# Optimization experiments

Measured on AMD Instinct MI355X. Metric: run time of the kernel, lower is better.

The kernel has to match this reference:

```python
import jax, jax.numpy as jnp
import numpy as np

STATE_LEN = 512
DIM_KEY = 128


def _rope(t, offset):
    # t: (b, h, s, d) -> rotate-half RoPE with given position offset
    b, h, s, d = t.shape
    inv_freq = 1.0 / (10000.0 ** (jnp.arange(0, d, 2, dtype=jnp.float32) / d))
    pos = jnp.arange(s, dtype=jnp.float32) + offset
    ang = pos[:, None] * inv_freq[None, :]            # (s, d/2)
    cos = jnp.concatenate([jnp.cos(ang), jnp.cos(ang)], axis=-1)  # (s, d)
    sin = jnp.concatenate([jnp.sin(ang), jnp.sin(ang)], axis=-1)
    t1, t2 = t[..., : d // 2], t[..., d // 2 :]
    rot = jnp.concatenate([-t2, t1], axis=-1)
    return t * cos + rot * sin


def _proj(x, w):
    # StackedLinear: mixes heads and features. x: (b,h,s,d), w: (h_in,h_out,d_in,d_out)
    return jnp.einsum('bhsd,hgde->bgse', x, w)


def setup_inputs() -> dict:
    key = jax.random.key(0)
    ks = jax.random.split(key, 10)
    x = jax.random.normal(ks[0], (2, 8, 3072, 128), dtype=jnp.float32)
    wshape = (8, 8, 128, 128)
    names = ['Wq', 'Wk', 'Wv', 'Wqs', 'Wks', 'Wvs', 'Wqe', 'Wke', 'Wve']
    inp = {'x': x}
    for i, n in enumerate(names):
        inp[n] = jax.random.normal(ks[i + 1], wshape, dtype=jnp.float32) * 0.02
    inp['offset'] = 0
    return inp


def reference(x, Wq, Wk, Wv, Wqs, Wks, Wvs, Wqe, Wke, Wve, offset):
    # extract_state: front state, middle, end state along seq axis
    xs = x[:, :, :STATE_LEN]
    xm = x[:, :, STATE_LEN:-STATE_LEN]
    xe = x[:, :, -STATE_LEN:]

    q = jnp.concatenate([_proj(xs, Wqs), _proj(xm, Wq), _proj(xe, Wqe)], axis=2)
    k = jnp.concatenate([_proj(xs, Wks), _proj(xm, Wk), _proj(xe, Wke)], axis=2)
    v = jnp.concatenate([_proj(xs, Wvs), _proj(xm, Wv), _proj(xe, Wve)], axis=2)

    q = _rope(q, offset)
    k = _rope(k, offset)

    scores = jnp.einsum('bhqd,bhkd->bhqk', q, k) / (DIM_KEY ** 0.5)
    s = scores.shape[-1]
    mask = jnp.tril(jnp.ones((s, s), dtype=bool))
    scores = jnp.where(mask[None, None], scores, -jnp.inf)
    att = jax.nn.softmax(scores, axis=-1)
    return jnp.einsum('bhqk,bhkd->bhqd', att, v)
```

## Files before the change

### kernel.cpp

```cpp
#include <hip/hip_runtime.h>
#include <hip/hip_bf16.h>
#include <stdint.h>


typedef __bf16   bf16x8 __attribute__((ext_vector_type(8)));
typedef float    f32x4  __attribute__((ext_vector_type(4)));
typedef uint32_t u32x4  __attribute__((ext_vector_type(4)));
typedef uint32_t u32x2  __attribute__((ext_vector_type(2)));
typedef uint16_t u16x4  __attribute__((ext_vector_type(4)));

struct f2 { float c, s; };

#define SEQ   3072
#define NFRQ  64

__device__ const uint8_t TQT[84] = {
  3,4,5,6, 7,7,8,8,9,9,10,10, 11,11,11,12,12,12,13,13,13,14,14,14,
  15,15,15,15,16,16,16,16,17,17,17,17,18,18,18,18,
  19,19,19,19,19,20,20,20,20,20,21,21,21,21,21,22,22,22,22,22,
  23,23,23,23,23,23, 2,6,10,14,18,22, 1,5,9,13,17,21, 0,4,8,12,16,20 };
__device__ const uint8_t TC[84] = {
  0,0,0,0, 0,1,0,1,0,1,0,1, 0,1,2,0,1,2,0,1,2,0,1,2,
  0,1,2,3,0,1,2,3,0,1,2,3,0,1,2,3,
  0,1,2,3,4,0,1,2,3,4,0,1,2,3,4,0,1,2,3,4,
  0,1,2,3,4,5, 0,1,2,3,4,5, 0,1,2,3,4,5, 0,1,2,3,4,5 };
__device__ const uint8_t PT[24]  = {0,0,0,0,0,1,2,3,4,6,8,10,12,15,18,21,24,28,32,36,40,45,50,55};
__device__ const uint8_t CCT[24] = {0,1,2,3,4,6,8,10,12,15,18,21,24,28,32,36,40,45,50,55,60,66,72,78};

static __device__ __forceinline__ uint16_t f2bf(float f) {
  union { float f; uint32_t u; } v; v.f = f;
  uint32_t r = (v.u + 0x7FFFu + ((v.u >> 16) & 1u)) >> 16;
  return (uint16_t)r;
}
static __device__ __forceinline__ float bf2f(uint16_t u) {
  union { uint32_t u; float f; } v; v.u = ((uint32_t)u) << 16;
  return v.f;
}
static __device__ __forceinline__ bf16x8 ldlds(const uint16_t* base, int byteoff) {
  u32x4 t = *reinterpret_cast<const u32x4*>(reinterpret_cast<const char*>(base) + byteoff);
  return __builtin_bit_cast(bf16x8, t);
}
static __device__ __forceinline__ bf16x8 ldglb(const uint16_t* p) {
  u32x4 t = *reinterpret_cast<const u32x4*>(p);
  return __builtin_bit_cast(bf16x8, t);
}

__global__ __launch_bounds__(256) void rope_table_kernel(f2* tab, const int* offp) {
  int i = blockIdx.x * 256 + threadIdx.x;
  if (i >= SEQ * NFRQ) return;
  int s = i >> 6, f = i & 63;
  float pos = (float)(s + offp[0]);
  float inv = powf(10000.0f, -(float)(2 * f) / 128.0f);
  float ang = pos * inv;
  tab[i].c = cosf(ang);
  tab[i].s = sinf(ang);
}

__global__ __launch_bounds__(256) void conv_x_kernel(const float* __restrict__ x,
                                                     uint16_t* __restrict__ xb) {
  int i = blockIdx.x * 256 + threadIdx.x;
  int d4 = i & 31;
  int t  = i >> 5;
  int s  = t % 3072;
  int bh = t / 3072;
  int h  = bh & 7, b = bh >> 3;
  f32x4 v = reinterpret_cast<const f32x4*>(x)[i];
  u16x4 o = { f2bf(v[0]), f2bf(v[1]), f2bf(v[2]), f2bf(v[3]) };
  size_t dst = ((size_t)(b * 3072 + s)) * 1024 + h * 128 + d4 * 4;
  *reinterpret_cast<u16x4*>(xb + dst) = o;
}

__global__ __launch_bounds__(256) void trans_w_kernel(
    const float* W0, const float* W1, const float* W2,
    const float* W3, const float* W4, const float* W5,
    const float* W6, const float* W7, const float* W8,
    uint16_t* __restrict__ Wt) {
  const float* Wall[9] = { W0, W1, W2, W3, W4, W5, W6, W7, W8 };
  int blk  = blockIdx.x;
  int widx = blk >> 6;
  int hg   = blk & 63;
  int h = hg >> 3, g = hg & 7;
  int qkv = widx / 3, seg = widx % 3;
  int sel = (seg == 0) ? (3 + qkv) : ((seg == 1) ? qkv : (6 + qkv));
  const float* src = Wall[sel] + (((size_t)h * 8 + g) * 128) * 128;
  uint16_t* dst = Wt + (((size_t)widx * 8 + g) * 128) * 1024 + h * 128;

  __shared__ uint16_t T[128 * 129];
  int tid = threadIdx.x;
  #pragma unroll
  for (int i = 0; i < 16; ++i) {
    int idx = tid + i * 256;
    int d = idx >> 5, e4 = idx & 31;
    f32x4 v = *reinterpret_cast<const f32x4*>(src + d * 128 + e4 * 4);
    int base = d * 129 + e4 * 4;
    T[base + 0] = f2bf(v[0]); T[base + 1] = f2bf(v[1]);
    T[base + 2] = f2bf(v[2]); T[base + 3] = f2bf(v[3]);
  }
  __syncthreads();
  #pragma unroll
  for (int i = 0; i < 8; ++i) {
    int idx = tid + i * 256;
    int e = idx >> 4, c = idx & 15, d0 = c * 8;
    uint32_t w0 = (uint32_t)T[(d0 + 0) * 129 + e] | ((uint32_t)T[(d0 + 1) * 129 + e] << 16);
    uint32_t w1 = (uint32_t)T[(d0 + 2) * 129 + e] | ((uint32_t)T[(d0 + 3) * 129 + e] << 16);
    uint32_t w2 = (uint32_t)T[(d0 + 4) * 129 + e] | ((uint32_t)T[(d0 + 5) * 129 + e] << 16);
    uint32_t w3 = (uint32_t)T[(d0 + 6) * 129 + e] | ((uint32_t)T[(d0 + 7) * 129 + e] << 16);
    u32x4 o = { w0, w1, w2, w3 };
    *reinterpret_cast<u32x4*>(dst + (size_t)e * 1024 + d0) = o;
  }
}

__global__ __launch_bounds__(256) void proj_kernel(
    const uint16_t* __restrict__ xb, const uint16_t* __restrict__ Wt,
    const f2* __restrict__ rtab,
    uint16_t* __restrict__ qb, uint16_t* __restrict__ kb,
    uint16_t* __restrict__ vtb) {
  const int bid = blockIdx.x;
  const int qkv = bid / 384;
  const int rem = bid % 384;
  const int mt  = rem >> 3;
  const int g   = rem & 7;
  const int R0  = mt * 128;
  const int b   = R0 / 3072;
  const int s0  = R0 % 3072;
  const int seg = (s0 < 512) ? 0 : ((s0 < 2560) ? 1 : 2);

  const uint16_t* Ag = xb + (size_t)R0 * 1024;
  const uint16_t* Bg = Wt + (((size_t)(qkv * 3 + seg) * 8 + g) << 17);

  __shared__ __align__(16) uint16_t Al[128 * 64];
  __shared__ __align__(16) uint16_t Bl[128 * 64];

  const int tid  = threadIdx.x;
  const int lane = tid & 63;
  const int w    = tid >> 6;
  const int l15  = lane & 15;
  const int l4   = lane >> 4;

  f32x4 acc[2][8];
  #pragma unroll
  for (int rf = 0; rf < 2; ++rf)
    #pragma unroll
    for (int nf = 0; nf < 8; ++nf) acc[rf][nf] = (f32x4){0.f, 0.f, 0.f, 0.f};

  for (int k0 = 0; k0 < 1024; k0 += 64) {
    #pragma unroll
    for (int i = 0; i < 4; ++i) {
      int idx = tid + i * 256;
      int r = idx >> 3, c8 = idx & 7;
      int off = (r * 128 + c8 * 16) ^ ((r & 7) << 4);
      u32x4 va = *reinterpret_cast<const u32x4*>(Ag + (size_t)r * 1024 + k0 + c8 * 8);
      *reinterpret_cast<u32x4*>(reinterpret_cast<char*>(Al) + off) = va;
      u32x4 vb = *reinterpret_cast<const u32x4*>(Bg + (size_t)r * 1024 + k0 + c8 * 8);
      *reinterpret_cast<u32x4*>(reinterpret_cast<char*>(Bl) + off) = vb;
    }
    __syncthreads();

    bf16x8 af[2][2];
    #pragma unroll
    for (int rf = 0; rf < 2; ++rf)
      #pragma unroll
      for (int kf = 0; kf < 2; ++kf) {
        int row = w * 32 + rf * 16 + l15;
        af[rf][kf] = ldlds(Al, (row * 128 + kf * 64 + l4 * 16) ^ ((row & 7) << 4));
      }
    #pragma unroll
    for (int nf = 0; nf < 8; ++nf) {
      int row = nf * 16 + l15;
      bf16x8 b0 = ldlds(Bl, (row * 128 + 0  + l4 * 16) ^ ((row & 7) << 4));
      bf16x8 b1 = ldlds(Bl, (row * 128 + 64 + l4 * 16) ^ ((row & 7) << 4));
      #pragma unroll
      for (int rf = 0; rf < 2; ++rf) {
        acc[rf][nf] = __builtin_amdgcn_mfma_f32_16x16x32_bf16(af[rf][0], b0, acc[rf][nf], 0, 0, 0);
        acc[rf][nf] = __builtin_amdgcn_mfma_f32_16x16x32_bf16(af[rf][1], b1, acc[rf][nf], 0, 0, 0);
      }
    }
    __syncthreads();
  }

  const int bg = b * 8 + g;
  if (qkv == 2) {
    #pragma unroll
    for (int rf = 0; rf < 2; ++rf)
      #pragma unroll
      for (int nf = 0; nf < 8; ++nf) {
        int e = nf * 16 + l15;
        int s = s0 + w * 32 + rf * 16 + l4 * 4;
        u16x4 pk = { f2bf(acc[rf][nf][0]), f2bf(acc[rf][nf][1]),
                     f2bf(acc[rf][nf][2]), f2bf(acc[rf][nf][3]) };
        *reinterpret_cast<u16x4*>(vtb + ((size_t)bg * 128 + e) * 3072 + s) = pk;
      }
  } else {
    uint16_t* outp = (qkv == 0) ? qb : kb;
    const float scl = (qkv == 0) ? 0.08838834764831845f : 1.0f;
    #pragma unroll
    for (int rf = 0; rf < 2; ++rf)
      #pragma unroll
      for (int j = 0; j < 4; ++j) {
        int s = s0 + w * 32 + rf * 16 + l4 * 4 + j;
        size_t rowb = ((size_t)bg * 3072 + s) * 128;
        #pragma unroll
        for (int nf = 0; nf < 4; ++nf) {
          int f = nf * 16 + l15;
          f2 cs = rtab[s * 64 + f];
          float q1 = acc[rf][nf][j], q2 = acc[rf][nf + 4][j];
          outp[rowb + f]      = f2bf((q1 * cs.c - q2 * cs.s) * scl);
          outp[rowb + 64 + f] = f2bf((q2 * cs.c + q1 * cs.s) * scl);
        }
      }
  }
}

__global__ __launch_bounds__(256) void attn_kernel(
    const uint16_t* __restrict__ qb, const uint16_t* __restrict__ kb,
    const uint16_t* __restrict__ vtb, float* __restrict__ out,
    uint16_t* __restrict__ opart, float* __restrict__ lsum) {
  const int bid = blockIdx.x;
  const int bg  = bid & 15;
  const int idx = bid >> 4;
  const int qt  = TQT[idx];
  const int c   = TC[idx];
  const int q0  = qt * 128;
  const int nkv = 2 * qt + 2;
  const int t0  = c * 8;
  const int t1  = (t0 + 8 < nkv) ? (t0 + 8) : nkv;

  const uint16_t* Qp = qb  + (size_t)bg * 3072 * 128;
  const uint16_t* Kp = kb  + (size_t)bg * 3072 * 128;
  const uint16_t* Vp = vtb + (size_t)bg * 128 * 3072;

  __shared__ __align__(16) uint16_t Kl[2][64 * 128];
  __shared__ __align__(16) uint16_t Vl[128 * 64];
  __shared__ __align__(16) uint16_t Pl[128 * 64];

  const int tid  = threadIdx.x;
  const int lane = tid & 63;
  const int w    = tid >> 6;
  const int l15  = lane & 15;
  const int l4   = lane >> 4;
  const int wrow = w * 32;

  bf16x8 aq[2][4];
  #pragma unroll
  for (int rf = 0; rf < 2; ++rf)
    #pragma unroll
    for (int kf = 0; kf < 4; ++kf) {
      int row = q0 + wrow + rf * 16 + l15;
      aq[rf][kf] = ldglb(Qp + (size_t)row * 128 + kf * 32 + l4 * 8);
    }

  f32x4 acc[2][8];
  #pragma unroll
  for (int rf = 0; rf < 2; ++rf)
    #pragma unroll
    for (int ef = 0; ef < 8; ++ef) acc[rf][ef] = (f32x4){0.f, 0.f, 0.f, 0.f};
  float lrow[2] = {0.f, 0.f};

  u32x4 kreg[4], vreg[4];
  {
    const int k0 = t0 * 64;
    #pragma unroll
    for (int i = 0; i < 4; ++i) {
      int id2 = tid + i * 256;
      kreg[i] = *reinterpret_cast<const u32x4*>(Kp + (size_t)(k0 + (id2 >> 4)) * 128 + (id2 & 15) * 8);
      vreg[i] = *reinterpret_cast<const u32x4*>(Vp + (size_t)(id2 >> 3) * 3072 + k0 + (id2 & 7) * 8);
    }
    #pragma unroll
    for (int i = 0; i < 4; ++i) {
      int id2 = tid + i * 256;
      int r = id2 >> 4, cc = id2 & 15;
      *reinterpret_cast<u32x4*>(reinterpret_cast<char*>(Kl[0]) +
          ((r * 256 + cc * 16) ^ ((r & 7) << 4))) = kreg[i];
      int e = id2 >> 3, c8 = id2 & 7;
      *reinterpret_cast<u32x4*>(reinterpret_cast<char*>(Vl) +
          ((e * 128 + c8 * 16) ^ ((e & 7) << 4))) = vreg[i];
    }
  }

  for (int t = t0; t < t1; ++t) {
    const int lt = (t - t0) & 1;
    __syncthreads();
    const bool more = (t + 1 < t1);
    if (more) {
      const int k0n = (t + 1) * 64;
      #pragma unroll
      for (int i = 0; i < 4; ++i) {
        int id2 = tid + i * 256;
        kreg[i] = *reinterpret_cast<const u32x4*>(Kp + (size_t)(k0n + (id2 >> 4)) * 128 + (id2 & 15) * 8);
        vreg[i] = *reinterpret_cast<const u32x4*>(Vp + (size_t)(id2 >> 3) * 3072 + k0n + (id2 & 7) * 8);
      }
    }

    const int k0 = t * 64;
    if (k0 <= q0 + wrow + 31) {
      f32x4 sc[2][4];
      #pragma unroll
      for (int rf = 0; rf < 2; ++rf)
        #pragma unroll
        for (int nf = 0; nf < 4; ++nf) sc[rf][nf] = (f32x4){0.f, 0.f, 0.f, 0.f};

      #pragma unroll
      for (int nf = 0; nf < 4; ++nf) {
        int row = nf * 16 + l15;
        #pragma unroll
        for (int kf = 0; kf < 4; ++kf) {
          bf16x8 bk = ldlds(Kl[lt], (row * 256 + kf * 64 + l4 * 16) ^ ((row & 7) << 4));
          #pragma unroll
          for (int rf = 0; rf < 2; ++rf)
            sc[rf][nf] = __builtin_amdgcn_mfma_f32_16x16x32_bf16(bk, aq[rf][kf], sc[rf][nf], 0, 0, 0);
        }
      }

      if (k0 + 63 > q0 + wrow) {
        #pragma unroll
        for (int rf = 0; rf < 2; ++rf)
          #pragma unroll
          for (int nf = 0; nf < 4; ++nf)
            #pragma unroll
            for (int j = 0; j < 4; ++j) {
              int qr = q0 + wrow + rf * 16 + l15;
              int kc = k0 + nf * 16 + l4 * 4 + j;
              if (kc > qr) sc[rf][nf][j] = -1.0e30f;
            }
      }

      #pragma unroll
      for (int rf = 0; rf < 2; ++rf) {
        int qr = wrow + rf * 16 + l15;
        int rowb = qr * 128;
        int swz = (qr & 7) << 4;
        #pragma unroll
        for (int nf = 0; nf < 4; ++nf) {
          uint16_t pb0 = f2bf(__expf(sc[rf][nf][0] - 3.0f));
          uint16_t pb1 = f2bf(__expf(sc[rf][nf][1] - 3.0f));
          uint16_t pb2 = f2bf(__expf(sc[rf][nf][2] - 3.0f));
          uint16_t pb3 = f2bf(__expf(sc[rf][nf][3] - 3.0f));
          lrow[rf] += bf2f(pb0) + bf2f(pb1) + bf2f(pb2) + bf2f(pb3);
          u32x2 dw = { (uint32_t)pb0 | ((uint32_t)pb1 << 16),
                       (uint32_t)pb2 | ((uint32_t)pb3 << 16) };
          *reinterpret_cast<u32x2*>(reinterpret_cast<char*>(Pl) +
              ((rowb + nf * 32 + l4 * 8) ^ swz)) = dw;
        }
      }

      bf16x8 ap[2][2];
      #pragma unroll
      for (int rf = 0; rf < 2; ++rf)
        #pragma unroll
        for (int kf = 0; kf < 2; ++kf) {
          int row = wrow + rf * 16 + l15;
          ap[rf][kf] = ldlds(Pl, (row * 128 + kf * 64 + l4 * 16) ^ ((row & 7) << 4));
        }
      #pragma unroll
      for (int ef = 0; ef < 8; ++ef) {
        int e = ef * 16 + l15;
        bf16x8 bv0 = ldlds(Vl, (e * 128 + 0  + l4 * 16) ^ ((e & 7) << 4));
        bf16x8 bv1 = ldlds(Vl, (e * 128 + 64 + l4 * 16) ^ ((e & 7) << 4));
        #pragma unroll
        for (int rf = 0; rf < 2; ++rf) {
          acc[rf][ef] = __builtin_amdgcn_mfma_f32_16x16x32_bf16(ap[rf][0], bv0, acc[rf][ef], 0, 0, 0);
          acc[rf][ef] = __builtin_amdgcn_mfma_f32_16x16x32_bf16(ap[rf][1], bv1, acc[rf][ef], 0, 0, 0);
        }
      }
    }

    if (more) {
      #pragma unroll
      for (int i = 0; i < 4; ++i) {
        int id2 = tid + i * 256;
        int r = id2 >> 4, cc = id2 & 15;
        *reinterpret_cast<u32x4*>(reinterpret_cast<char*>(Kl[lt ^ 1]) +
            ((r * 256 + cc * 16) ^ ((r & 7) << 4))) = kreg[i];
      }
      __syncthreads();
      #pragma unroll
      for (int i = 0; i < 4; ++i) {
        int id2 = tid + i * 256;
        int e = id2 >> 3, c8 = id2 & 7;
        *reinterpret_cast<u32x4*>(reinterpret_cast<char*>(Vl) +
            ((e * 128 + c8 * 16) ^ ((e & 7) << 4))) = vreg[i];
      }
    }
  }

  const int lidx = bg * 84 + CCT[qt] + c;
  #pragma unroll
  for (int rf = 0; rf < 2; ++rf) {
    float ps = lrow[rf];
    ps += __shfl_xor(ps, 16);
    ps += __shfl_xor(ps, 32);
    if (l4 == 0)
      lsum[(size_t)lidx * 128 + wrow + rf * 16 + l15] = ps;
  }
  if (c == 0) {
    float* obase = out + ((size_t)bg * 3072 + q0) * 128;
    #pragma unroll
    for (int rf = 0; rf < 2; ++rf)
      #pragma unroll
      for (int j = 0; j < 4; ++j) {
        int rl = wrow + rf * 16 + l4 * 4 + j;
        #pragma unroll
        for (int ef = 0; ef < 8; ++ef)
          obase[(size_t)rl * 128 + ef * 16 + l15] = acc[rf][ef][j];
      }
  } else {
    int slot = bg * 60 + PT[qt] + (c - 1);
    uint16_t* pbase = opart + (size_t)slot * 16384;
    #pragma unroll
    for (int rf = 0; rf < 2; ++rf)
      #pragma unroll
      for (int j = 0; j < 4; ++j) {
        int rl = wrow + rf * 16 + l4 * 4 + j;
        #pragma unroll
        for (int ef = 0; ef < 8; ++ef)
          pbase[rl * 128 + ef * 16 + l15] = f2bf(acc[rf][ef][j]);
      }
  }
}

__global__ __launch_bounds__(256) void combine_kernel(
    float* __restrict__ out, const uint16_t* __restrict__ opart,
    const float* __restrict__ lsum) {
  const int bid = blockIdx.x;
  const int bg = bid / 24, qt = bid % 24;
  const int nc = (qt >> 2) + 1;
  const int lbase = bg * 84 + CCT[qt];
  const int pbase = bg * 60 + PT[qt];
  const int t = threadIdx.x;
  const int r = t >> 1, half = t & 1;

  float l = 0.f;
  for (int c2 = 0; c2 < nc; ++c2)
    l += lsum[(size_t)(lbase + c2) * 128 + r];
  float inv = 1.0f / l;

  float* orow = out + ((size_t)bg * 3072 + qt * 128 + r) * 128 + half * 64;
  f32x4 a[16];
  #pragma unroll
  for (int v = 0; v < 16; ++v)
    a[v] = reinterpret_cast<const f32x4*>(orow)[v];
  for (int c2 = 1; c2 < nc; ++c2) {
    const uint16_t* p = opart + (size_t)(pbase + c2 - 1) * 16384 + r * 128 + half * 64;
    #pragma unroll
    for (int v = 0; v < 16; ++v) {
      u16x4 pk = reinterpret_cast<const u16x4*>(p)[v];
      a[v] += (f32x4){ bf2f(pk[0]), bf2f(pk[1]), bf2f(pk[2]), bf2f(pk[3]) };
    }
  }
  #pragma unroll
  for (int v = 0; v < 16; ++v)
    reinterpret_cast<f32x4*>(orow)[v] = a[v] * inv;
}

extern "C" void kernel_launch(void* const* d_in, const int* in_sizes, int n_in,
                              void* d_out, int out_size, void* d_ws, size_t ws_size,
                              hipStream_t stream) {
  const float* x = (const float*)d_in[0];
  const float* W[9];
  for (int i = 0; i < 9; ++i) W[i] = (const float*)d_in[1 + i];
  const int* offset = (const int*)d_in[10];
  float* out = (float*)d_out;

  char* ws = (char*)d_ws;
  f2*       rtab  = (f2*)(ws + 0);
  uint16_t* xb    = (uint16_t*)(ws + 1572864);
  uint16_t* Wt    = (uint16_t*)(ws + 14155776);
  uint16_t* qb    = (uint16_t*)(ws + 33030144);
  uint16_t* kb    = (uint16_t*)(ws + 45613056);
  uint16_t* vtb   = (uint16_t*)(ws + 58195968);
  uint16_t* opart = (uint16_t*)(ws + 0);
  float*    lsum  = (float*)(ws + 31457280);

  hipLaunchKernelGGL(rope_table_kernel, dim3(768),  dim3(256), 0, stream, rtab, offset);
  hipLaunchKernelGGL(conv_x_kernel,     dim3(6144), dim3(256), 0, stream, x, xb);
  hipLaunchKernelGGL(trans_w_kernel,    dim3(576),  dim3(256), 0, stream,
                     W[0], W[1], W[2], W[3], W[4], W[5], W[6], W[7], W[8], Wt);
  hipLaunchKernelGGL(proj_kernel,       dim3(1152), dim3(256), 0, stream,
                     xb, Wt, rtab, qb, kb, vtb);
  hipLaunchKernelGGL(attn_kernel,       dim3(1344), dim3(256), 0, stream,
                     qb, kb, vtb, out, opart, lsum);
  hipLaunchKernelGGL(combine_kernel,    dim3(384),  dim3(256), 0, stream,
                     out, opart, lsum);
}
```

Before: 229.6 us.

## Single-buffer K tile, add occupancy hint, use packed bf16 convert in attention

Drops the double-buffered K tile in LDS (from 64 KB to 48 KB per block) so more blocks fit per CU, and adds a launch-bounds minimum of 3 blocks per SM. Both K and V are now written after one barrier once compute finishes. The manual bf16 rounding of the softmax probabilities is replaced by the hardware v_cvt_pk_bf16_f32 packed convert. The cost is that K stores can no longer overlap the previous tile's compute, and the register cap from the occupancy hint may cause spills.

```diff
diff --git a/kernel.cpp b/kernel.cpp
--- a/kernel.cpp
+++ b/kernel.cpp
@@ -35,6 +35,11 @@
 static __device__ __forceinline__ float bf2f(uint16_t u) {
   union { uint32_t u; float f; } v; v.u = ((uint32_t)u) << 16;
   return v.f;
+}
+static __device__ __forceinline__ uint32_t cvt_pk_bf16(float a, float b) {
+  uint32_t r;
+  asm("v_cvt_pk_bf16_f32 %0, %1, %2" : "=v"(r) : "v"(a), "v"(b));
+  return r;
 }
 static __device__ __forceinline__ bf16x8 ldlds(const uint16_t* base, int byteoff) {
   u32x4 t = *reinterpret_cast<const u32x4*>(reinterpret_cast<const char*>(base) + byteoff);
@@ -211,7 +216,7 @@
   }
 }
 
-__global__ __launch_bounds__(256) void attn_kernel(
+__global__ __launch_bounds__(256, 3) void attn_kernel(
     const uint16_t* __restrict__ qb, const uint16_t* __restrict__ kb,
     const uint16_t* __restrict__ vtb, float* __restrict__ out,
     uint16_t* __restrict__ opart, float* __restrict__ lsum) {
@@ -229,7 +234,7 @@
   const uint16_t* Kp = kb  + (size_t)bg * 3072 * 128;
   const uint16_t* Vp = vtb + (size_t)bg * 128 * 3072;
 
-  __shared__ __align__(16) uint16_t Kl[2][64 * 128];
+  __shared__ __align__(16) uint16_t Kl[64 * 128];
   __shared__ __align__(16) uint16_t Vl[128 * 64];
   __shared__ __align__(16) uint16_t Pl[128 * 64];
 
@@ -269,7 +274,7 @@
     for (int i = 0; i < 4; ++i) {
       int id2 = tid + i * 256;
       int r = id2 >> 4, cc = id2 & 15;
-      *reinterpret_cast<u32x4*>(reinterpret_cast<char*>(Kl[0]) +
+      *reinterpret_cast<u32x4*>(reinterpret_cast<char*>(Kl) +
           ((r * 256 + cc * 16) ^ ((r & 7) << 4))) = kreg[i];
       int e = id2 >> 3, c8 = id2 & 7;
       *reinterpret_cast<u32x4*>(reinterpret_cast<char*>(Vl) +
@@ -278,7 +283,6 @@
   }
 
   for (int t = t0; t < t1; ++t) {
-    const int lt = (t - t0) & 1;
     __syncthreads();
     const bool more = (t + 1 < t1);
     if (more) {
@@ -304,7 +308,7 @@
         int row = nf * 16 + l15;
         #pragma unroll
         for (int kf = 0; kf < 4; ++kf) {
-          bf16x8 bk = ldlds(Kl[lt], (row * 256 + kf * 64 + l4 * 16) ^ ((row & 7) << 4));
+          bf16x8 bk = ldlds(Kl, (row * 256 + kf * 64 + l4 * 16) ^ ((row & 7) << 4));
           #pragma unroll
           for (int rf = 0; rf < 2; ++rf)
             sc[rf][nf] = __builtin_amdgcn_mfma_f32_16x16x32_bf16(bk, aq[rf][kf], sc[rf][nf], 0, 0, 0);
@@ -331,13 +335,17 @@
         int swz = (qr & 7) << 4;
         #pragma unroll
         for (int nf = 0; nf < 4; ++nf) {
-          uint16_t pb0 = f2bf(__expf(sc[rf][nf][0] - 3.0f));
-          uint16_t pb1 = f2bf(__expf(sc[rf][nf][1] - 3.0f));
-          uint16_t pb2 = f2bf(__expf(sc[rf][nf][2] - 3.0f));
-          uint16_t pb3 = f2bf(__expf(sc[rf][nf][3] - 3.0f));
-          lrow[rf] += bf2f(pb0) + bf2f(pb1) + bf2f(pb2) + bf2f(pb3);
-          u32x2 dw = { (uint32_t)pb0 | ((uint32_t)pb1 << 16),
-                       (uint32_t)pb2 | ((uint32_t)pb3 << 16) };
+          float p0 = __expf(sc[rf][nf][0] - 3.0f);
+          float p1 = __expf(sc[rf][nf][1] - 3.0f);
+          float p2 = __expf(sc[rf][nf][2] - 3.0f);
+          float p3 = __expf(sc[rf][nf][3] - 3.0f);
+          uint32_t dw0 = cvt_pk_bf16(p0, p1);
+          uint32_t dw1 = cvt_pk_bf16(p2, p3);
+          lrow[rf] += __builtin_bit_cast(float, dw0 << 16)
+                    + __builtin_bit_cast(float, dw0 & 0xffff0000u)
+                    + __builtin_bit_cast(float, dw1 << 16)
+                    + __builtin_bit_cast(float, dw1 & 0xffff0000u);
+          u32x2 dw = { dw0, dw1 };
           *reinterpret_cast<u32x2*>(reinterpret_cast<char*>(Pl) +
               ((rowb + nf * 32 + l4 * 8) ^ swz)) = dw;
         }
@@ -365,17 +373,13 @@
     }
 
     if (more) {
+      __syncthreads();
       #pragma unroll
       for (int i = 0; i < 4; ++i) {
         int id2 = tid + i * 256;
         int r = id2 >> 4, cc = id2 & 15;
-        *reinterpret_cast<u32x4*>(reinterpret_cast<char*>(Kl[lt ^ 1]) +
+        *reinterpret_cast<u32x4*>(reinterpret_cast<char*>(Kl) +
             ((r * 256 + cc * 16) ^ ((r & 7) << 4))) = kreg[i];
-      }
-      __syncthreads();
-      #pragma unroll
-      for (int i = 0; i < 4; ++i) {
-        int id2 = tid + i * 256;
         int e = id2 >> 3, c8 = id2 & 7;
         *reinterpret_cast<u32x4*>(reinterpret_cast<char*>(Vl) +
             ((e * 128 + c8 * 16) ^ ((e & 7) << 4))) = vreg[i];
```

New measurement: 405.7 us. 1.77x slower.
